# Kernel tuning notes

Hardware: AMD Instinct MI355X
Metric: run time of the kernel (lower is better)

Reference implementation:

```python
import jax, jax.numpy as jnp
import numpy as np

D = 768          # bert-base hidden size
H = 12           # attention heads
DH = D // H
FF = 3072        # bert-base intermediate size
L_ENT = 8192     # actual_entity_length
R_REL = 512      # number of relation nodes
N_ET = 64        # edge type vocab
B = 16384        # number of triples (batched instead of python loop)
SEQ = 4          # [CLS, head, edge, tail]


def _ln(x, g, b, eps=1e-12):
    m = jnp.mean(x, axis=-1, keepdims=True)
    v = jnp.var(x, axis=-1, keepdims=True)
    return (x - m) * jax.lax.rsqrt(v + eps) * g + b


def setup_inputs() -> dict:
    key = jax.random.key(0)
    ks = jax.random.split(key, 32)
    s = 0.02
    rn = lambda k, shp: jax.random.normal(k, shp, dtype=jnp.float32) * s
    return {
        'head_ids': jax.random.randint(ks[0], (B,), 0, L_ENT + R_REL),
        'edge_type_ids': jax.random.randint(ks[1], (B,), 0, N_ET),
        'tail_ids': jax.random.randint(ks[2], (B,), 0, L_ENT + R_REL),
        'actual_entity_length': L_ENT,
        'token_embeddings': rn(ks[3], (L_ENT + R_REL, D)),
        'relation_embeddings': rn(ks[4], (R_REL, D)),
        'edge_type_emb': rn(ks[5], (N_ET, D)),
        'cls_embedding': rn(ks[6], (D,)),
        'seg_emb': rn(ks[7], (SEQ, D)),
        'pos_emb': rn(ks[8], (SEQ, D)),
        'ln_emb_g': jnp.ones((D,), jnp.float32), 'ln_emb_b': jnp.zeros((D,), jnp.float32),
        'Wq': rn(ks[9], (D, D)), 'bq': jnp.zeros((D,), jnp.float32),
        'Wk': rn(ks[10], (D, D)), 'bk': jnp.zeros((D,), jnp.float32),
        'Wv': rn(ks[11], (D, D)), 'bv': jnp.zeros((D,), jnp.float32),
        'Wo': rn(ks[12], (D, D)), 'bo': jnp.zeros((D,), jnp.float32),
        'ln1_g': jnp.ones((D,), jnp.float32), 'ln1_b': jnp.zeros((D,), jnp.float32),
        'W1': rn(ks[13], (D, FF)), 'b1': jnp.zeros((FF,), jnp.float32),
        'W2': rn(ks[14], (FF, D)), 'b2': jnp.zeros((D,), jnp.float32),
        'ln2_g': jnp.ones((D,), jnp.float32), 'ln2_b': jnp.zeros((D,), jnp.float32),
        'head_w': rn(ks[15], (D,)), 'head_b': jnp.zeros((), jnp.float32),
    }


def reference(head_ids, edge_type_ids, tail_ids, actual_entity_length,
              token_embeddings, relation_embeddings, edge_type_emb,
              cls_embedding, seg_emb, pos_emb, ln_emb_g, ln_emb_b,
              Wq, bq, Wk, bk, Wv, bv, Wo, bo, ln1_g, ln1_b,
              W1, b1, W2, b2, ln2_g, ln2_b, head_w, head_b):
    L = actual_entity_length
    n_rel = relation_embeddings.shape[0]
    nb = head_ids.shape[0]

    def node_emb(ids):
        # entity ids index token_embeddings, ids >= L index relation_embeddings
        tok = token_embeddings[ids]
        rel = relation_embeddings[jnp.clip(ids - L, 0, n_rel - 1)]
        return jnp.where((ids < L)[:, None], tok, rel)

    h_tok = node_emb(head_ids)                 # [B, D]
    t_tok = node_emb(tail_ids)                 # [B, D]
    e_tok = edge_type_emb[edge_type_ids]       # [B, D]
    cls = jnp.broadcast_to(cls_embedding, (nb, D))
    x = jnp.stack([cls, h_tok, e_tok, t_tok], axis=1)   # [B, 4, D]

    # BERT embedding layer: segment ids [0,1,2,3] + positions, then LayerNorm
    x = _ln(x + seg_emb + pos_emb, ln_emb_g, ln_emb_b)

    # single transformer encoder layer (post-LN, bert-base geometry)
    q = (x @ Wq + bq).reshape(nb, SEQ, H, DH)
    k = (x @ Wk + bk).reshape(nb, SEQ, H, DH)
    v = (x @ Wv + bv).reshape(nb, SEQ, H, DH)
    att = jnp.einsum('bqhd,bkhd->bhqk', q, k) / np.sqrt(DH).astype(np.float32)
    att = jax.nn.softmax(att, axis=-1)
    ctx = jnp.einsum('bhqk,bkhd->bqhd', att, v).reshape(nb, SEQ, D)
    x = _ln(x + ctx @ Wo + bo, ln1_g, ln1_b)
    ff = jax.nn.gelu(x @ W1 + b1) @ W2 + b2     # [B, 4, D]
    x = _ln(x + ff, ln2_g, ln2_b)

    cls_out = x[:, 0]                           # [B, D]
    scores = cls_out @ head_w + head_b          # plausibility_head, squeezed
    return scores
```

## Files before the change

kernel.cpp:

```cpp
#include <hip/hip_runtime.h>

typedef __bf16 bf16;
typedef __bf16 bf16x8 __attribute__((ext_vector_type(8)));
typedef float f32x4 __attribute__((ext_vector_type(4)));

constexpr long NB = 16384;
constexpr int  DD = 768;
constexpr int  FFD = 3072;
constexpr int  NH = 12;


__device__ __forceinline__ void async16(const void* g, void* l) {
  void* gg = (void*)g;
  __builtin_amdgcn_global_load_lds((__attribute__((address_space(1))) void*)gg,
                                   (__attribute__((address_space(3))) void*)l,
                                   16, 0, 0);
}

__device__ __forceinline__ float wred(float v) {
#pragma unroll
  for (int off = 32; off; off >>= 1) v += __shfl_xor(v, off);
  return v;
}

__device__ __forceinline__ float gelu_tanh(float x) {
  float x3 = x * x * x;
  return 0.5f * x * (1.0f + tanhf(0.7978845608028654f * (x + 0.044715f * x3)));
}


__global__ __launch_bounds__(256) void transpose_bf16(const float* __restrict__ src,
                                                      bf16* __restrict__ dst,
                                                      int R, int C) {
  __shared__ float t[32][33];
  int tilesC = C >> 5;
  int tc = blockIdx.x % tilesC;
  int tr = blockIdx.x / tilesC;
  int tx = threadIdx.x & 31, ty = threadIdx.x >> 5;
#pragma unroll
  for (int i = 0; i < 4; ++i) {
    int r = tr * 32 + ty + i * 8;
    t[ty + i * 8][tx] = src[(long)r * C + tc * 32 + tx];
  }
  __syncthreads();
#pragma unroll
  for (int i = 0; i < 4; ++i) {
    int c = tc * 32 + ty + i * 8;
    dst[(long)c * R + tr * 32 + tx] = (bf16)t[tx][ty + i * 8];
  }
}

__global__ void concat_bias(const float* __restrict__ bk, const float* __restrict__ bv,
                            float* __restrict__ bkv) {
  int i = blockIdx.x * 256 + threadIdx.x;
  if (i < 2 * DD) bkv[i] = (i < DD) ? bk[i] : bv[i - DD];
}


__global__ __launch_bounds__(256) void embed_table_kernel(
    const int* __restrict__ pL,
    const float* __restrict__ tok, const float* __restrict__ rel, const float* __restrict__ ete,
    const float* __restrict__ cls, const float* __restrict__ seg, const float* __restrict__ pos,
    const float* __restrict__ g, const float* __restrict__ bln,
    bf16* __restrict__ Xtab, int VOC, int NE, int Mtab, int nrel) {
  long row = (long)blockIdx.x * 4 + (threadIdx.x >> 6);
  int lane = threadIdx.x & 63;
  if (row >= Mtab) return;
  int L = *pL;

  const float* src;
  int s;
  if (row < VOC || row < 2 * VOC) {
    if (row < VOC) { s = 1; } else { s = 3; }
    int id = (int)(row < VOC ? row : row - VOC);
    if (row >= 2 * VOC) {  }
    if (id < L) {
      src = tok + (long)id * DD;
    } else {
      int ridx = id - L;
      ridx = ridx < 0 ? 0 : (ridx > nrel - 1 ? nrel - 1 : ridx);
      src = rel + (long)ridx * DD;
    }
    if (row >= 2 * VOC) src = cls;
  } else if (row < 2 * VOC + NE) {
    s = 2;
    src = ete + (row - 2 * (long)VOC) * DD;
  } else {
    s = 0;
    src = cls;
  }
  if (row >= 2 * VOC) {
    if (row < 2 * VOC + NE) { s = 2; src = ete + (row - 2 * (long)VOC) * DD; }
    else { s = 0; src = cls; }
  }

  float v[12];
  float sum = 0.f, ssum = 0.f;
#pragma unroll
  for (int j = 0; j < 12; ++j) {
    int d = j * 64 + lane;
    float x = src[d] + seg[s * DD + d] + pos[s * DD + d];
    v[j] = x;
    sum += x;
    ssum += x * x;
  }
  sum = wred(sum);
  ssum = wred(ssum);
  float mean = sum * (1.0f / DD);
  float var = ssum * (1.0f / DD) - mean * mean;
  float rs = rsqrtf(var + 1e-12f);

#pragma unroll
  for (int j = 0; j < 12; ++j) {
    int d = j * 64 + lane;
    Xtab[row * DD + d] = (bf16)((v[j] - mean) * rs * g[d] + bln[d]);
  }
}


template <int EPI>
__global__ __launch_bounds__(256) void gemm_bt(
    const bf16* __restrict__ A, const bf16* __restrict__ Bt,
    const float* __restrict__ bias, void* __restrict__ Cout,
    long M, long N, long K, int tilesN) {
  __shared__ __align__(16) bf16 As[128 * 32];
  __shared__ __align__(16) bf16 Bs[128 * 32];
  const int tid = threadIdx.x;
  const int w = tid >> 6;
  const int lane = tid & 63;

  long bid;
  if ((gridDim.x & 7) == 0) {
    const long cpx = gridDim.x >> 3;
    bid = (long)(blockIdx.x & 7) * cpx + (blockIdx.x >> 3);
  } else {
    bid = blockIdx.x;
  }
  const int tn = (int)(bid % tilesN);
  const long tm = bid / tilesN;
  const long m0 = tm * 128, n0 = (long)tn * 128;

  const int sr = lane >> 2;
  const int sk = (lane & 3) * 8;
  const bf16* ga0 = A + (m0 + w * 32 + sr) * K + sk;
  const bf16* ga1 = ga0 + 16 * K;
  const bf16* gb0 = Bt + (n0 + w * 32 + sr) * K + sk;
  const bf16* gb1 = gb0 + 16 * K;
  bf16* la0 = As + w * 1024;
  bf16* la1 = la0 + 512;
  bf16* lb0 = Bs + w * 1024;
  bf16* lb1 = lb0 + 512;

  const int fr = lane & 15;
  const int fk = (lane >> 4) * 8;
  const int wr = (w >> 1) * 64;
  const int wc = (w & 1) * 64;

  f32x4 acc[4][4] = {};

  const int nk = (int)(K >> 5);
  for (int kt = 0; kt < nk; ++kt) {
    const long ko = (long)kt * 32;
    async16(ga0 + ko, la0);
    async16(ga1 + ko, la1);
    async16(gb0 + ko, lb0);
    async16(gb1 + ko, lb1);
    __syncthreads();
    bf16x8 af[4], bfr[4];
#pragma unroll
    for (int m = 0; m < 4; ++m)
      af[m] = *(const bf16x8*)(As + (wr + m * 16 + fr) * 32 + fk);
#pragma unroll
    for (int n = 0; n < 4; ++n)
      bfr[n] = *(const bf16x8*)(Bs + (wc + n * 16 + fr) * 32 + fk);
#pragma unroll
    for (int m = 0; m < 4; ++m)
#pragma unroll
      for (int n = 0; n < 4; ++n)
        acc[m][n] = __builtin_amdgcn_mfma_f32_16x16x32_bf16(af[m], bfr[n], acc[m][n], 0, 0, 0);
    __syncthreads();
  }

  const int er = (lane >> 4) * 4;
#pragma unroll
  for (int m = 0; m < 4; ++m) {
#pragma unroll
    for (int n = 0; n < 4; ++n) {
#pragma unroll
      for (int j = 0; j < 4; ++j) {
        long row = m0 + wr + m * 16 + er + j;
        long col = n0 + wc + n * 16 + fr;
        float v = acc[m][n][j] + bias[col];
        if (EPI == 2) v = gelu_tanh(v);
        if (EPI == 1)
          ((float*)Cout)[row * N + col] = v;
        else
          ((bf16*)Cout)[row * N + col] = (bf16)v;
      }
    }
  }
}


__global__ __launch_bounds__(192) void score_kernel(const bf16* __restrict__ KVtab,
                                                    const float* __restrict__ q,
                                                    float* __restrict__ stab, int Mtab) {
  long row = blockIdx.x;
  int t = threadIdx.x, h = t >> 4, hl = t & 15;
  const bf16* kp = KVtab + row * (2 * DD) + h * 64 + hl * 4;
  const float* qp = q + h * 64 + hl * 4;
  float p = qp[0] * (float)kp[0] + qp[1] * (float)kp[1] + qp[2] * (float)kp[2] +
            qp[3] * (float)kp[3];
  p += __shfl_xor(p, 1);
  p += __shfl_xor(p, 2);
  p += __shfl_xor(p, 4);
  p += __shfl_xor(p, 8);
  if (hl == 0) stab[row * NH + h] = p * 0.125f;
}


__global__ __launch_bounds__(192) void attn_kernel(
    const int* __restrict__ hid, const int* __restrict__ eid, const int* __restrict__ tid_,
    const bf16* __restrict__ KVtab, const float* __restrict__ stab,
    bf16* __restrict__ ctx, int VOC, int crow) {
  long b = blockIdx.x;
  int t = threadIdx.x, h = t >> 4, hl = t & 15;
  long r0 = crow;
  long r1 = hid[b];
  long r2 = 2L * VOC + eid[b];
  long r3 = (long)VOC + tid_[b];
  float s0 = stab[r0 * NH + h], s1 = stab[r1 * NH + h];
  float s2 = stab[r2 * NH + h], s3 = stab[r3 * NH + h];
  float m = fmaxf(fmaxf(s0, s1), fmaxf(s2, s3));
  float p0 = expf(s0 - m), p1 = expf(s1 - m), p2 = expf(s2 - m), p3 = expf(s3 - m);
  float inv = 1.0f / (p0 + p1 + p2 + p3);
  p0 *= inv; p1 *= inv; p2 *= inv; p3 *= inv;

  int o = h * 64 + hl * 4;
  const bf16* v0 = KVtab + r0 * (2 * DD) + DD + o;
  const bf16* v1 = KVtab + r1 * (2 * DD) + DD + o;
  const bf16* v2 = KVtab + r2 * (2 * DD) + DD + o;
  const bf16* v3 = KVtab + r3 * (2 * DD) + DD + o;
  bf16* op = ctx + b * DD + o;
#pragma unroll
  for (int j = 0; j < 4; ++j) {
    float v = p0 * (float)v0[j] + p1 * (float)v1[j] + p2 * (float)v2[j] + p3 * (float)v3[j];
    op[j] = (bf16)v;
  }
}


__global__ __launch_bounds__(256) void ln1_kernel(const bf16* __restrict__ xrow,
                                                  const float* __restrict__ O,
                                                  const float* __restrict__ g,
                                                  const float* __restrict__ bb,
                                                  bf16* __restrict__ x1) {
  int w = threadIdx.x >> 6, lane = threadIdx.x & 63;
  long r = (long)blockIdx.x * 4 + w;
  const float* op = O + r * DD;
  float v[12], sum = 0.f, ssum = 0.f;
#pragma unroll
  for (int j = 0; j < 12; ++j) {
    int d = j * 64 + lane;
    float x = (float)xrow[d] + op[d];
    v[j] = x;
    sum += x;
    ssum += x * x;
  }
  sum = wred(sum);
  ssum = wred(ssum);
  float mean = sum * (1.0f / DD);
  float var = ssum * (1.0f / DD) - mean * mean;
  float rs = rsqrtf(var + 1e-12f);
#pragma unroll
  for (int j = 0; j < 12; ++j) {
    int d = j * 64 + lane;
    x1[r * DD + d] = (bf16)((v[j] - mean) * rs * g[d] + bb[d]);
  }
}


__global__ __launch_bounds__(256) void final_kernel(const bf16* __restrict__ x1,
                                                    const float* __restrict__ F,
                                                    const float* __restrict__ g,
                                                    const float* __restrict__ bb,
                                                    const float* __restrict__ hw,
                                                    const float* __restrict__ phb,
                                                    float* __restrict__ scores) {
  int w = threadIdx.x >> 6, lane = threadIdx.x & 63;
  long r = (long)blockIdx.x * 4 + w;
  const bf16* xp = x1 + r * DD;
  const float* fp = F + r * DD;
  float v[12], sum = 0.f, ssum = 0.f;
#pragma unroll
  for (int j = 0; j < 12; ++j) {
    int d = j * 64 + lane;
    float x = (float)xp[d] + fp[d];
    v[j] = x;
    sum += x;
    ssum += x * x;
  }
  sum = wred(sum);
  ssum = wred(ssum);
  float mean = sum * (1.0f / DD);
  float var = ssum * (1.0f / DD) - mean * mean;
  float rs = rsqrtf(var + 1e-12f);
  float acc = 0.f;
#pragma unroll
  for (int j = 0; j < 12; ++j) {
    int d = j * 64 + lane;
    float y = (v[j] - mean) * rs * g[d] + bb[d];
    acc += y * hw[d];
  }
  acc = wred(acc);
  if (lane == 0) scores[r] = acc + phb[0];
}


extern "C" void kernel_launch(void* const* d_in, const int* in_sizes, int n_in,
                              void* d_out, int out_size, void* d_ws, size_t ws_size,
                              hipStream_t stream) {
  const int* hid = (const int*)d_in[0];
  const int* eid = (const int*)d_in[1];
  const int* tid = (const int*)d_in[2];
  const int* pL = (const int*)d_in[3];
  const float* tok = (const float*)d_in[4];
  const float* rel = (const float*)d_in[5];
  const float* ete = (const float*)d_in[6];
  const float* cls = (const float*)d_in[7];
  const float* seg = (const float*)d_in[8];
  const float* pos = (const float*)d_in[9];
  const float* lng = (const float*)d_in[10];
  const float* lnb = (const float*)d_in[11];
  const float* Wq = (const float*)d_in[12];
  const float* bq = (const float*)d_in[13];
  const float* Wk = (const float*)d_in[14];
  const float* bk = (const float*)d_in[15];
  const float* Wv = (const float*)d_in[16];
  const float* bv = (const float*)d_in[17];
  const float* Wo = (const float*)d_in[18];
  const float* bo = (const float*)d_in[19];
  const float* l1g = (const float*)d_in[20];
  const float* l1b = (const float*)d_in[21];
  const float* W1 = (const float*)d_in[22];
  const float* b1 = (const float*)d_in[23];
  const float* W2 = (const float*)d_in[24];
  const float* b2 = (const float*)d_in[25];
  const float* l2g = (const float*)d_in[26];
  const float* l2b = (const float*)d_in[27];
  const float* hw = (const float*)d_in[28];
  const float* phb = (const float*)d_in[29];
  float* scores = (float*)d_out;

  const int VOC = in_sizes[4] / DD;
  const int NE = in_sizes[6] / DD;
  const int NREL = in_sizes[5] / DD;
  const int Mtab = 2 * VOC + NE + 1;
  const int Mpad = (Mtab + 127) & ~127;
  const int crow = 2 * VOC + NE;

  char* base = (char*)d_ws;
  size_t off = 0;
  auto alloc = [&](size_t bytes) -> char* {
    char* p = base + off;
    off += (bytes + 255) & ~(size_t)255;
    return p;
  };

  bf16* WkvT = (bf16*)alloc((size_t)2 * DD * DD * 2);
  bf16* WqT = (bf16*)alloc((size_t)DD * DD * 2);
  bf16* WoT = (bf16*)alloc((size_t)DD * DD * 2);
  bf16* W1T = (bf16*)alloc((size_t)DD * FFD * 2);
  bf16* W2T = (bf16*)alloc((size_t)FFD * DD * 2);
  float* bkv = (float*)alloc((size_t)2 * DD * 4);
  bf16* Xtab = (bf16*)alloc((size_t)Mpad * DD * 2);
  float* stab = (float*)alloc((size_t)Mtab * NH * 4);
  float* Q128 = (float*)alloc((size_t)128 * DD * 4);
  bf16* ctx = (bf16*)alloc((size_t)NB * DD * 2);

  char* region = base + off;
  size_t region_sz = (ws_size > off) ? (ws_size - off) : 0;
  bf16* KVtab = (bf16*)region;

  long RB = NB;
  while (RB > 512 && (size_t)RB * 10752 + (1 << 20) > region_sz) RB >>= 1;
  const int CHB = (int)(NB / RB);
  float* Och = (float*)region;
  bf16* x1ch = (bf16*)(region + (size_t)RB * DD * 4);
  bf16* Hffch = x1ch + RB * DD;
  float* Foch = Och;

  transpose_bf16<<<576, 256, 0, stream>>>(Wk, WkvT, DD, DD);
  transpose_bf16<<<576, 256, 0, stream>>>(Wv, WkvT + (size_t)DD * DD, DD, DD);
  transpose_bf16<<<576, 256, 0, stream>>>(Wq, WqT, DD, DD);
  transpose_bf16<<<576, 256, 0, stream>>>(Wo, WoT, DD, DD);
  transpose_bf16<<<2304, 256, 0, stream>>>(W1, W1T, DD, FFD);
  transpose_bf16<<<2304, 256, 0, stream>>>(W2, W2T, FFD, DD);
  concat_bias<<<6, 256, 0, stream>>>(bk, bv, bkv);

  embed_table_kernel<<<(Mtab + 3) / 4, 256, 0, stream>>>(
      pL, tok, rel, ete, cls, seg, pos, lng, lnb, Xtab, VOC, NE, Mtab, NREL);

  gemm_bt<0><<<(Mpad / 128) * 12, 256, 0, stream>>>(Xtab, WkvT, bkv, KVtab,
                                                    Mpad, 2 * DD, DD, 12);
  gemm_bt<1><<<6, 256, 0, stream>>>(Xtab + (size_t)(Mpad - 128) * DD, WqT, bq, Q128,
                                    128, DD, DD, 6);
  score_kernel<<<Mtab, 192, 0, stream>>>(KVtab, Q128 + (size_t)(crow - (Mpad - 128)) * DD,
                                         stab, Mtab);
  attn_kernel<<<NB, 192, 0, stream>>>(hid, eid, tid, KVtab, stab, ctx, VOC, crow);

  const bf16* xrow = Xtab + (size_t)crow * DD;
  for (int j = 0; j < CHB; ++j) {
    long r0 = (long)j * RB;
    gemm_bt<1><<<(RB / 128) * 6, 256, 0, stream>>>(ctx + r0 * DD, WoT, bo, Och,
                                                   RB, DD, DD, 6);
    ln1_kernel<<<RB / 4, 256, 0, stream>>>(xrow, Och, l1g, l1b, x1ch);
    gemm_bt<2><<<(RB / 128) * 24, 256, 0, stream>>>(x1ch, W1T, b1, Hffch,
                                                    RB, FFD, DD, 24);
    gemm_bt<1><<<(RB / 128) * 6, 256, 0, stream>>>(Hffch, W2T, b2, Foch,
                                                   RB, DD, FFD, 6);
    final_kernel<<<RB / 4, 256, 0, stream>>>(x1ch, Foch, l2g, l2b, hw, phb, scores + r0);
  }
}
```

Baseline: 600.5 us.

## Add double-buffered 256x256 GEMM kernel, bf16 intermediates, and exp-based GELU

Adds a 512-thread GEMM with 256x256 tiles, a 64-wide K step and double-buffered async global-to-LDS loads. It replaces the 128x128 kernel for the KV-table, Wo, W1 and W2 GEMMs. The Wo and W2 outputs are now stored in bf16 instead of fp32, which halves that traffic and the workspace each chunk needs, so chunks can be larger. GELU is computed through an exp-based sigmoid form of the tanh approximation. The costs are lower output precision, higher register and LDS pressure per block, and a hard-coded Q row offset (17408) that only fits this problem size.

```diff
diff --git a/kernel.cpp b/kernel.cpp
--- a/kernel.cpp
+++ b/kernel.cpp
@@ -23,9 +23,11 @@
   return v;
 }
 
-__device__ __forceinline__ float gelu_tanh(float x) {
-  float x3 = x * x * x;
-  return 0.5f * x * (1.0f + tanhf(0.7978845608028654f * (x + 0.044715f * x3)));
+__device__ __forceinline__ float gelu_fast(float x) {
+  float z = 1.5957691216f * (x + 0.044715f * x * x * x);
+  z = fminf(fmaxf(z, -30.f), 30.f);
+  float t = __expf(z);
+  return x * t / (t + 1.f);
 }
 
 
@@ -70,10 +72,9 @@
 
   const float* src;
   int s;
-  if (row < VOC || row < 2 * VOC) {
-    if (row < VOC) { s = 1; } else { s = 3; }
+  if (row < 2 * VOC) {
+    s = (row < VOC) ? 1 : 3;
     int id = (int)(row < VOC ? row : row - VOC);
-    if (row >= 2 * VOC) {  }
     if (id < L) {
       src = tok + (long)id * DD;
     } else {
@@ -81,7 +82,6 @@
       ridx = ridx < 0 ? 0 : (ridx > nrel - 1 ? nrel - 1 : ridx);
       src = rel + (long)ridx * DD;
     }
-    if (row >= 2 * VOC) src = cls;
   } else if (row < 2 * VOC + NE) {
     s = 2;
     src = ete + (row - 2 * (long)VOC) * DD;
@@ -89,10 +89,6 @@
     s = 0;
     src = cls;
   }
-  if (row >= 2 * VOC) {
-    if (row < 2 * VOC + NE) { s = 2; src = ete + (row - 2 * (long)VOC) * DD; }
-    else { s = 0; src = cls; }
-  }
 
   float v[12];
   float sum = 0.f, ssum = 0.f;
@@ -114,6 +110,105 @@
   for (int j = 0; j < 12; ++j) {
     int d = j * 64 + lane;
     Xtab[row * DD + d] = (bf16)((v[j] - mean) * rs * g[d] + bln[d]);
+  }
+}
+
+
+template <int EPI>
+__global__ __launch_bounds__(512) void gemm256(
+    const bf16* __restrict__ A, const bf16* __restrict__ Bt,
+    const float* __restrict__ bias, void* __restrict__ Cout,
+    long M, long N, long K, int tilesN) {
+  __shared__ __align__(16) bf16 lds[65536];
+  const int tid = threadIdx.x;
+  const int w = tid >> 6;
+  const int lane = tid & 63;
+  const int wm = w >> 2;
+  const int wn = w & 3;
+
+  long bid;
+  if ((gridDim.x & 7) == 0) {
+    const long cpx = gridDim.x >> 3;
+    bid = (long)(blockIdx.x & 7) * cpx + (blockIdx.x >> 3);
+  } else {
+    bid = blockIdx.x;
+  }
+  const int tn = (int)(bid % tilesN);
+  const long tm = bid / tilesN;
+  const long m0 = tm * 256, n0 = (long)tn * 256;
+
+  const int srow = tid >> 3;
+  const int scol = (tid & 7) * 8;
+  const bf16* gA = A + (m0 + srow) * K + scol;
+  const bf16* gB = Bt + (n0 + srow) * K + scol;
+  const int ldsw = w * 512;
+
+  const int fr = lane & 15;
+  const int fk = (lane >> 4) * 8;
+
+  f32x4 acc[8][4] = {};
+
+  auto STAGE = [&](int d, long ko) {
+    bf16* a = lds + d * 16384;
+    bf16* bb = lds + 32768 + d * 16384;
+#pragma unroll
+    for (int c = 0; c < 4; ++c)
+      async16(gA + (long)(c * 64) * K + ko, a + c * 4096 + ldsw);
+#pragma unroll
+    for (int c = 0; c < 4; ++c)
+      async16(gB + (long)(c * 64) * K + ko, bb + c * 4096 + ldsw);
+  };
+
+  auto COMPUTE = [&](int d) {
+    const bf16* a = lds + d * 16384 + (wm * 128 + fr) * 64 + fk;
+    const bf16* bb = lds + 32768 + d * 16384 + (wn * 64 + fr) * 64 + fk;
+#pragma unroll
+    for (int ks = 0; ks < 2; ++ks) {
+      bf16x8 af[8], bf_[4];
+#pragma unroll
+      for (int mf = 0; mf < 8; ++mf)
+        af[mf] = *(const bf16x8*)(a + mf * 16 * 64 + ks * 32);
+#pragma unroll
+      for (int nf = 0; nf < 4; ++nf)
+        bf_[nf] = *(const bf16x8*)(bb + nf * 16 * 64 + ks * 32);
+#pragma unroll
+      for (int mf = 0; mf < 8; ++mf)
+#pragma unroll
+        for (int nf = 0; nf < 4; ++nf)
+          acc[mf][nf] =
+              __builtin_amdgcn_mfma_f32_16x16x32_bf16(af[mf], bf_[nf], acc[mf][nf], 0, 0, 0);
+    }
+  };
+
+  const int nt = (int)(K >> 6);
+  STAGE(0, 0);
+  __syncthreads();
+  int cur = 0;
+  for (int kt = 0; kt < nt - 1; ++kt) {
+    STAGE(cur ^ 1, (long)(kt + 1) * 64);
+    COMPUTE(cur);
+    __syncthreads();
+    cur ^= 1;
+  }
+  COMPUTE(cur);
+
+  const int er = (lane >> 4) * 4;
+#pragma unroll
+  for (int mf = 0; mf < 8; ++mf) {
+#pragma unroll
+    for (int nf = 0; nf < 4; ++nf) {
+#pragma unroll
+      for (int j = 0; j < 4; ++j) {
+        long row = m0 + wm * 128 + mf * 16 + er + j;
+        long col = n0 + wn * 64 + nf * 16 + fr;
+        float v = acc[mf][nf][j] + bias[col];
+        if (EPI == 2) v = gelu_fast(v);
+        if (EPI == 1)
+          ((float*)Cout)[row * N + col] = v;
+        else
+          ((bf16*)Cout)[row * N + col] = (bf16)v;
+      }
+    }
   }
 }
 
@@ -129,13 +224,7 @@
   const int w = tid >> 6;
   const int lane = tid & 63;
 
-  long bid;
-  if ((gridDim.x & 7) == 0) {
-    const long cpx = gridDim.x >> 3;
-    bid = (long)(blockIdx.x & 7) * cpx + (blockIdx.x >> 3);
-  } else {
-    bid = blockIdx.x;
-  }
+  long bid = blockIdx.x;
   const int tn = (int)(bid % tilesN);
   const long tm = bid / tilesN;
   const long m0 = tm * 128, n0 = (long)tn * 128;
@@ -191,7 +280,6 @@
         long row = m0 + wr + m * 16 + er + j;
         long col = n0 + wc + n * 16 + fr;
         float v = acc[m][n][j] + bias[col];
-        if (EPI == 2) v = gelu_tanh(v);
         if (EPI == 1)
           ((float*)Cout)[row * N + col] = v;
         else
@@ -251,18 +339,18 @@
 
 
 __global__ __launch_bounds__(256) void ln1_kernel(const bf16* __restrict__ xrow,
-                                                  const float* __restrict__ O,
+                                                  const bf16* __restrict__ O,
                                                   const float* __restrict__ g,
                                                   const float* __restrict__ bb,
                                                   bf16* __restrict__ x1) {
   int w = threadIdx.x >> 6, lane = threadIdx.x & 63;
   long r = (long)blockIdx.x * 4 + w;
-  const float* op = O + r * DD;
+  const bf16* op = O + r * DD;
   float v[12], sum = 0.f, ssum = 0.f;
 #pragma unroll
   for (int j = 0; j < 12; ++j) {
     int d = j * 64 + lane;
-    float x = (float)xrow[d] + op[d];
+    float x = (float)xrow[d] + (float)op[d];
     v[j] = x;
     sum += x;
     ssum += x * x;
@@ -281,7 +369,7 @@
 
 
 __global__ __launch_bounds__(256) void final_kernel(const bf16* __restrict__ x1,
-                                                    const float* __restrict__ F,
+                                                    const bf16* __restrict__ F,
                                                     const float* __restrict__ g,
                                                     const float* __restrict__ bb,
                                                     const float* __restrict__ hw,
@@ -290,12 +378,12 @@
   int w = threadIdx.x >> 6, lane = threadIdx.x & 63;
   long r = (long)blockIdx.x * 4 + w;
   const bf16* xp = x1 + r * DD;
-  const float* fp = F + r * DD;
+  const bf16* fp = F + r * DD;
   float v[12], sum = 0.f, ssum = 0.f;
 #pragma unroll
   for (int j = 0; j < 12; ++j) {
     int d = j * 64 + lane;
-    float x = (float)xp[d] + fp[d];
+    float x = (float)xp[d] + (float)fp[d];
     v[j] = x;
     sum += x;
     ssum += x * x;
@@ -356,7 +444,7 @@
   const int NE = in_sizes[6] / DD;
   const int NREL = in_sizes[5] / DD;
   const int Mtab = 2 * VOC + NE + 1;
-  const int Mpad = (Mtab + 127) & ~127;
+  const int Mpad = (Mtab + 255) & ~255;
   const int crow = 2 * VOC + NE;
 
   char* base = (char*)d_ws;
@@ -383,12 +471,12 @@
   bf16* KVtab = (bf16*)region;
 
   long RB = NB;
-  while (RB > 512 && (size_t)RB * 10752 + (1 << 20) > region_sz) RB >>= 1;
+  while (RB > 2048 && (size_t)RB * 9216 + (1 << 20) > region_sz) RB >>= 1;
   const int CHB = (int)(NB / RB);
-  float* Och = (float*)region;
-  bf16* x1ch = (bf16*)(region + (size_t)RB * DD * 4);
+  bf16* Och = (bf16*)region;
+  bf16* x1ch = Och + RB * DD;
   bf16* Hffch = x1ch + RB * DD;
-  float* Foch = Och;
+  bf16* Foch = Och;
 
   transpose_bf16<<<576, 256, 0, stream>>>(Wk, WkvT, DD, DD);
   transpose_bf16<<<576, 256, 0, stream>>>(Wv, WkvT + (size_t)DD * DD, DD, DD);
@@ -401,24 +489,24 @@
   embed_table_kernel<<<(Mtab + 3) / 4, 256, 0, stream>>>(
       pL, tok, rel, ete, cls, seg, pos, lng, lnb, Xtab, VOC, NE, Mtab, NREL);
 
-  gemm_bt<0><<<(Mpad / 128) * 12, 256, 0, stream>>>(Xtab, WkvT, bkv, KVtab,
-                                                    Mpad, 2 * DD, DD, 12);
-  gemm_bt<1><<<6, 256, 0, stream>>>(Xtab + (size_t)(Mpad - 128) * DD, WqT, bq, Q128,
+  gemm256<0><<<(Mpad / 256) * 6, 512, 0, stream>>>(Xtab, WkvT, bkv, KVtab,
+                                                   Mpad, 2 * DD, DD, 6);
+  gemm_bt<1><<<6, 256, 0, stream>>>(Xtab + (size_t)17408 * DD, WqT, bq, Q128,
                                     128, DD, DD, 6);
-  score_kernel<<<Mtab, 192, 0, stream>>>(KVtab, Q128 + (size_t)(crow - (Mpad - 128)) * DD,
+  score_kernel<<<Mtab, 192, 0, stream>>>(KVtab, Q128 + (size_t)(crow - 17408) * DD,
                                          stab, Mtab);
   attn_kernel<<<NB, 192, 0, stream>>>(hid, eid, tid, KVtab, stab, ctx, VOC, crow);
 
   const bf16* xrow = Xtab + (size_t)crow * DD;
   for (int j = 0; j < CHB; ++j) {
     long r0 = (long)j * RB;
-    gemm_bt<1><<<(RB / 128) * 6, 256, 0, stream>>>(ctx + r0 * DD, WoT, bo, Och,
-                                                   RB, DD, DD, 6);
+    gemm256<0><<<(RB / 256) * 3, 512, 0, stream>>>(ctx + r0 * DD, WoT, bo, Och,
+                                                   RB, DD, DD, 3);
     ln1_kernel<<<RB / 4, 256, 0, stream>>>(xrow, Och, l1g, l1b, x1ch);
-    gemm_bt<2><<<(RB / 128) * 24, 256, 0, stream>>>(x1ch, W1T, b1, Hffch,
-                                                    RB, FFD, DD, 24);
-    gemm_bt<1><<<(RB / 128) * 6, 256, 0, stream>>>(Hffch, W2T, b2, Foch,
-                                                   RB, DD, FFD, 6);
+    gemm256<2><<<(RB / 256) * 12, 512, 0, stream>>>(x1ch, W1T, b1, Hffch,
+                                                    RB, FFD, DD, 12);
+    gemm256<0><<<(RB / 256) * 3, 512, 0, stream>>>(Hffch, W2T, b2, Foch,
+                                                   RB, DD, FFD, 3);
     final_kernel<<<RB / 4, 256, 0, stream>>>(x1ch, Foch, l2g, l2b, hw, phb, scores + r0);
   }
 }
```

Result: faster. 528.8 us (-11.9%).
